# Optimization experiments

Measured on AMD Instinct MI355X. Metric: run time of the kernel, lower is better.

Reference implementation:

```python
import jax, jax.numpy as jnp
import numpy as np

SDF_W = 7000.0
EIK_W = 600.0
ORI_W = 500.0
NEAR_ORI_W = 10.0
GRADN_W = 200.0
K_NEIGHBORS = 2


def _orientation_sign(query, surface, normals, k=K_NEIGHBORS):
    # Original detaches to numpy for a scipy KDTree query -> stop_gradient here.
    q = jax.lax.stop_gradient(query)       # [Q,3]
    s = jax.lax.stop_gradient(surface)     # [S,3]
    n = jax.lax.stop_gradient(normals)     # [S,3]
    # Brute-force squared distances [Q,S] (GEMM-dominated).
    d2 = (jnp.sum(q * q, axis=-1, keepdims=True)
          - 2.0 * (q @ s.T)
          + jnp.sum(s * s, axis=-1)[None, :])
    _, idx = jax.lax.top_k(-d2, k)         # [Q,k] nearest-neighbor indices
    near_pts = s[idx]                      # [Q,k,3]
    near_nrm = n[idx]                      # [Q,k,3]
    vecs = q[:, None, :] - near_pts        # [Q,k,3]
    dots = jnp.sum(vecs * near_nrm, axis=-1)  # [Q,k]
    return jnp.sign(jnp.mean(dots, axis=1))   # [Q]


def setup_inputs() -> dict:
    key = jax.random.key(0)
    ks = jax.random.split(key, 8)
    N = 16384
    return {
        "manifold_pred": jax.random.normal(ks[0], (N, 1), jnp.float32) * 0.1,
        "manifold_grad": jax.random.normal(ks[1], (N, 3), jnp.float32),
        "nonmanifold_pred": jax.random.normal(ks[2], (N, 1), jnp.float32),
        "near_points_pred": jax.random.normal(ks[3], (N, 1), jnp.float32) * 0.1,
        "surface_points": jax.random.normal(ks[4], (N, 3), jnp.float32),
        "surface_normals": jax.random.normal(ks[5], (N, 3), jnp.float32),
        "off_surface_points": jax.random.normal(ks[6], (N, 3), jnp.float32) * 1.5,
        "near_points": jax.random.normal(ks[7], (N, 3), jnp.float32),
    }


def reference(manifold_pred, manifold_grad, nonmanifold_pred, near_points_pred,
              surface_points, surface_normals, off_surface_points, near_points):
    sdf_loss = jnp.mean(manifold_pred ** 2)
    eikonal_loss = jnp.mean((jnp.linalg.norm(manifold_grad, axis=-1) - 1.0) ** 2)

    signs_off = _orientation_sign(off_surface_points, surface_points, surface_normals)
    orientation_loss = jnp.mean(jax.nn.relu(-nonmanifold_pred * signs_off[:, None]))

    signs_near = _orientation_sign(near_points, surface_points, surface_normals)
    near_surface_orientation_loss = jnp.mean(jax.nn.relu(-near_points_pred * signs_near[:, None]))

    gradient_normal_loss = jnp.mean((manifold_grad - surface_normals) ** 2)

    total = (SDF_W * sdf_loss + EIK_W * eikonal_loss + ORI_W * orientation_loss
             + NEAR_ORI_W * near_surface_orientation_loss + GRADN_W * gradient_normal_loss)
    return (total, sdf_loss, eikonal_loss, orientation_loss,
            near_surface_orientation_loss, gradient_normal_loss)
```

## Files before the change

### kernel.cpp

```cpp
#include <hip/hip_runtime.h>
#include <math.h>

#define SDF_W      7000.0f
#define EIK_W      600.0f
#define ORI_W      500.0f
#define NEAR_ORI_W 10.0f
#define GRADN_W    200.0f

#define TILE   2048
#define NWAVE  8
#define CHK    64
#define WS_STRIDE 512
#define WS_REC 4096


__device__ __forceinline__ float neg_half_norm2(float sx, float sy, float sz) {
    return -0.5f * fmaf(sx, sx, fmaf(sy, sy, sz * sz));
}
__device__ __forceinline__ float score(float qx, float qy, float qz,
                                       float sx, float sy, float sz, float nh) {
    return fmaf(qx, sx, fmaf(qy, sy, fmaf(qz, sz, nh)));
}

__global__ __launch_bounds__(512) void nn_scan(
    const float* __restrict__ offq, const float* __restrict__ nearq,
    const float* __restrict__ surf,
    float* __restrict__ ws, int S, int Qoff, int QT)
{
    __shared__ float4 tile[TILE];
    const int t    = threadIdx.x;
    const int lane = t & 63;
    const int wv   = __builtin_amdgcn_readfirstlane(t >> 6);

    const int qgroup = blockIdx.x >> 1;
    const int shalf  = blockIdx.x & 1;

    const int halfLen = (((S + 1) / 2) + (CHK - 1)) & ~(CHK - 1);
    const int sb = shalf ? (halfLen < S ? halfLen : S) : 0;
    const int se = shalf ? S : (halfLen < S ? halfLen : S);

    const int qA = qgroup * 128 + lane;
    const int qB = qA + 64;
    float qAx = 0.f, qAy = 0.f, qAz = 0.f, qBx = 0.f, qBy = 0.f, qBz = 0.f;
    if (qA < QT) {
        const float* p = (qA < Qoff) ? (offq + 3 * qA) : (nearq + 3 * (qA - Qoff));
        qAx = p[0]; qAy = p[1]; qAz = p[2];
    }
    if (qB < QT) {
        const float* p = (qB < Qoff) ? (offq + 3 * qB) : (nearq + 3 * (qB - Qoff));
        qBx = p[0]; qBy = p[1]; qBz = p[2];
    }

    float M1a = -3.0e38f, M2a = -3.0e38f, M1b = -3.0e38f, M2b = -3.0e38f;
    float P1a = M1a, P2a = M2a, P1b = M1b, P2b = M2b;
    int c1a = 0, c2a = 0, c1b = 0, c2b = 0;

    for (int base = sb; base < se; base += TILE) {
        __syncthreads();
        {
            int p0 = base + t * 4;
            if (p0 + 4 <= se) {
                const float4* g4 = (const float4*)(surf + 3 * p0);
                float4 r0 = g4[0], r1 = g4[1], r2 = g4[2];
                tile[t*4+0] = make_float4(r0.x, r0.y, r0.z, neg_half_norm2(r0.x, r0.y, r0.z));
                tile[t*4+1] = make_float4(r0.w, r1.x, r1.y, neg_half_norm2(r0.w, r1.x, r1.y));
                tile[t*4+2] = make_float4(r1.z, r1.w, r2.x, neg_half_norm2(r1.z, r1.w, r2.x));
                tile[t*4+3] = make_float4(r2.y, r2.z, r2.w, neg_half_norm2(r2.y, r2.z, r2.w));
            } else {
                #pragma unroll
                for (int k = 0; k < 4; ++k) {
                    int p = p0 + k;
                    if (p < se) {
                        float sx = surf[3*p], sy = surf[3*p+1], sz = surf[3*p+2];
                        tile[t*4+k] = make_float4(sx, sy, sz, neg_half_norm2(sx, sy, sz));
                    } else {
                        tile[t*4+k] = make_float4(0.f, 0.f, 0.f, -3.0e38f);
                    }
                }
            }
        }
        __syncthreads();
        const int lo = wv * (TILE / NWAVE);
        const float4* tp = tile + lo;
        const int ccbase = (base + lo) >> 6;
        #pragma unroll 1
        for (int c4 = 0; c4 < (TILE / NWAVE) / CHK; ++c4) {
            const float4* cp = tp + c4 * CHK;
            #pragma unroll 8
            for (int o = 0; o < CHK; ++o) {
                float4 s4 = cp[o];
                float ga = score(qAx, qAy, qAz, s4.x, s4.y, s4.z, s4.w);
                float ta = fminf(ga, M1a);
                M2a = fmaxf(M2a, ta);
                M1a = fmaxf(M1a, ga);
                float gb = score(qBx, qBy, qBz, s4.x, s4.y, s4.z, s4.w);
                float tb = fminf(gb, M1b);
                M2b = fmaxf(M2b, tb);
                M1b = fmaxf(M1b, gb);
            }
            int cid = ccbase + c4;
            c1a = (M1a != P1a) ? cid : c1a;  P1a = M1a;
            c2a = (M2a != P2a) ? cid : c2a;  P2a = M2a;
            c1b = (M1b != P1b) ? cid : c1b;  P1b = M1b;
            c2b = (M2b != P2b) ? cid : c2b;  P2b = M2b;
        }
    }

    __syncthreads();
    float4* rec = tile;
    rec[wv * 128 + lane]      = make_float4(M1a, M2a, __int_as_float(c1a), __int_as_float(c2a));
    rec[wv * 128 + 64 + lane] = make_float4(M1b, M2b, __int_as_float(c1b), __int_as_float(c2b));
    __syncthreads();
    if (t < 128) {
        float4 r = rec[t];
        float M1 = r.x, M2 = r.y;
        int c1 = __float_as_int(r.z), c2 = __float_as_int(r.w);
        #pragma unroll
        for (int w = 1; w < NWAVE; ++w) {
            float4 a = rec[w * 128 + t];
            float a1 = a.x, a2 = a.y;
            int ac1 = __float_as_int(a.z), ac2 = __float_as_int(a.w);
            if (a1 > M1)      { M2 = M1; c2 = c1; M1 = a1; c1 = ac1; }
            else if (a1 > M2) { M2 = a1; c2 = ac1; }
            if (a2 > M2)      { M2 = a2; c2 = ac2; }
        }
        int gq = qgroup * 128 + t;
        if (gq < QT) {
            ((float4*)(ws + WS_REC))[gq * 2 + shalf] =
                make_float4(M1, M2, __int_as_float(c1), __int_as_float(c2));
        }
    }
}

__device__ __forceinline__ int find_first(const float* __restrict__ surf, int S,
                                          int c, float qx, float qy, float qz,
                                          float target, int exclude)
{
    int j0 = c * CHK;
    int j1 = j0 + CHK; if (j1 > S) j1 = S;
    if (j1 - j0 == CHK) {
        const float4* g4 = (const float4*)(surf + 3 * j0);
        int found = -1;
        #pragma unroll 1
        for (int b = 0; b < CHK / 16 && found < 0; ++b) {
            float4 raw[12];
            #pragma unroll
            for (int k = 0; k < 12; ++k) raw[k] = g4[b * 12 + k];
            const float* f = (const float*)raw;
            #pragma unroll
            for (int p = 0; p < 16; ++p) {
                float sx = f[3*p], sy = f[3*p+1], sz = f[3*p+2];
                float g = score(qx, qy, qz, sx, sy, sz, neg_half_norm2(sx, sy, sz));
                int j = j0 + b * 16 + p;
                if (found < 0 && g == target && j != exclude) found = j;
            }
        }
        return found;
    }
    for (int j = j0; j < j1; ++j) {
        float sx = surf[3*j], sy = surf[3*j+1], sz = surf[3*j+2];
        float g = score(qx, qy, qz, sx, sy, sz, neg_half_norm2(sx, sy, sz));
        if (g == target && j != exclude) return j;
    }
    return -1;
}

__global__ __launch_bounds__(128) void recover_k(
    const float* __restrict__ offq, const float* __restrict__ nearq,
    const float* __restrict__ surf, const float* __restrict__ norms,
    const float* __restrict__ nmpred, const float* __restrict__ nppred,
    const float* __restrict__ mp, const float* __restrict__ mg,
    const float* __restrict__ sn,
    float* __restrict__ ws, int S, int Qoff, int QT, int N)
{
    const int t = threadIdx.x;
    const int q = blockIdx.x * 128 + t;

    float termOri = 0.f, termNori = 0.f;
    if (q < QT) {
        const float4* recs = (const float4*)(ws + WS_REC);
        float4 r0 = recs[q * 2 + 0], r1 = recs[q * 2 + 1];
        float M1 = r0.x, M2 = r0.y;
        int c1 = __float_as_int(r0.z), c2 = __float_as_int(r0.w);
        {
            float a1 = r1.x, a2 = r1.y;
            int ac1 = __float_as_int(r1.z), ac2 = __float_as_int(r1.w);
            if (a1 > M1)      { M2 = M1; c2 = c1; M1 = a1; c1 = ac1; }
            else if (a1 > M2) { M2 = a1; c2 = ac1; }
            if (a2 > M2)      { M2 = a2; c2 = ac2; }
        }
        bool isNear = (q >= Qoff);
        const float* qp = isNear ? (nearq + 3 * (q - Qoff)) : (offq + 3 * q);
        float qx = qp[0], qy = qp[1], qz = qp[2];

        int I1 = find_first(surf, S, c1, qx, qy, qz, M1, -1);
        if (I1 < 0) I1 = 0;
        int I2 = find_first(surf, S, c2, qx, qy, qz, M2, I1);
        if (I2 < 0) I2 = (I1 == 0 && S > 1) ? 1 : 0;

        float d1 = (qx - surf[3*I1]) * norms[3*I1]
                 + (qy - surf[3*I1+1]) * norms[3*I1+1]
                 + (qz - surf[3*I1+2]) * norms[3*I1+2];
        float d2 = (qx - surf[3*I2]) * norms[3*I2]
                 + (qy - surf[3*I2+1]) * norms[3*I2+1]
                 + (qz - surf[3*I2+2]) * norms[3*I2+2];
        float ms = d1 + d2;
        float sgn = (ms > 0.f) ? 1.f : ((ms < 0.f) ? -1.f : 0.f);
        float pred = isNear ? nppred[q - Qoff] : nmpred[q];
        float term = fmaxf(0.f, -pred * sgn);
        termOri  = isNear ? 0.f : term;
        termNori = isNear ? term : 0.f;
    }

    float sdf = 0.f, eik = 0.f, gn = 0.f;
    for (int i = q; i < N; i += QT) {
        float p = mp[i];
        sdf += p * p;
        float gx = mg[3*i], gy = mg[3*i+1], gz = mg[3*i+2];
        float nrm = sqrtf(fmaf(gx, gx, fmaf(gy, gy, gz * gz)));
        float d = nrm - 1.0f;
        eik += d * d;
        float nx = sn[3*i], ny = sn[3*i+1], nz = sn[3*i+2];
        float dx = gx - nx, dy = gy - ny, dz = gz - nz;
        gn += fmaf(dx, dx, fmaf(dy, dy, dz * dz));
    }

    __shared__ float red[5][128];
    red[0][t] = termOri; red[1][t] = termNori;
    red[2][t] = sdf;     red[3][t] = eik;      red[4][t] = gn;
    __syncthreads();
    for (int off = 64; off > 0; off >>= 1) {
        if (t < off) {
            #pragma unroll
            for (int k = 0; k < 5; ++k) red[k][t] += red[k][t + off];
        }
        __syncthreads();
    }
    if (t == 0) {
        #pragma unroll
        for (int k = 0; k < 5; ++k) ws[k * WS_STRIDE + blockIdx.x] = red[k][0];
    }
}

__global__ __launch_bounds__(256) void final_k(
    const float* __restrict__ ws, float* __restrict__ out,
    int N, int RB, int Qoff, int Qnear)
{
    __shared__ float r[5][256];
    int t = threadIdx.x;
    float s[5] = {0.f, 0.f, 0.f, 0.f, 0.f};
    for (int i = t; i < RB; i += 256) {
        #pragma unroll
        for (int k = 0; k < 5; ++k) s[k] += ws[k * WS_STRIDE + i];
    }
    #pragma unroll
    for (int k = 0; k < 5; ++k) r[k][t] = s[k];
    __syncthreads();
    for (int off = 128; off > 0; off >>= 1) {
        if (t < off) {
            #pragma unroll
            for (int k = 0; k < 5; ++k) r[k][t] += r[k][t + off];
        }
        __syncthreads();
    }
    if (t == 0) {
        float orim  = r[0][0] / (float)Qoff;
        float norim = r[1][0] / (float)Qnear;
        float sdfm  = r[2][0] / (float)N;
        float eikm  = r[3][0] / (float)N;
        float gnm   = r[4][0] / (3.0f * (float)N);
        out[0] = SDF_W * sdfm + EIK_W * eikm + ORI_W * orim
               + NEAR_ORI_W * norim + GRADN_W * gnm;
        out[1] = sdfm;
        out[2] = eikm;
        out[3] = orim;
        out[4] = norim;
        out[5] = gnm;
    }
}

extern "C" void kernel_launch(void* const* d_in, const int* in_sizes, int n_in,
                              void* d_out, int out_size, void* d_ws, size_t ws_size,
                              hipStream_t stream)
{
    const float* mp    = (const float*)d_in[0];
    const float* mg    = (const float*)d_in[1];
    const float* nmp   = (const float*)d_in[2];
    const float* npp   = (const float*)d_in[3];
    const float* sp    = (const float*)d_in[4];
    const float* sn    = (const float*)d_in[5];
    const float* offp  = (const float*)d_in[6];
    const float* nearp = (const float*)d_in[7];
    float* out = (float*)d_out;

    const int N     = in_sizes[0];
    const int S     = in_sizes[4] / 3;
    const int Qoff  = in_sizes[2];
    const int Qnear = in_sizes[3];
    const int QT    = Qoff + Qnear;

    float* ws = (float*)d_ws;

    const int qgroups = (QT + 127) / 128;
    const int RB      = (QT + 127) / 128;

    nn_scan<<<qgroups * 2, 512, 0, stream>>>(offp, nearp, sp, ws, S, Qoff, QT);
    recover_k<<<RB, 128, 0, stream>>>(offp, nearp, sp, sn, nmp, npp,
                                      mp, mg, sn, ws, S, Qoff, QT, N);
    final_k<<<1, 256, 0, stream>>>(ws, out, N, RB, Qoff, Qnear);
}
```

Before: 151.1 us.

## Scan four queries per lane with fmed3 top-2 and wave-parallel index recovery

The NN scan kernel now holds four query points per lane instead of two, so each shared-memory surface load is reused across more queries. The top-2 update is compressed into a single fmed3 plus a max. Recovery now gives each query a whole wavefront, which scores the 64 chunk candidates in parallel and selects the match by ballot instead of a serial per-thread search. The block reductions use wave shuffles. The risks are higher register pressure in the scan and half as many scan blocks (256 instead of 512), which lowers occupancy and CU coverage.

```diff
diff --git a/kernel.cpp b/kernel.cpp
--- a/kernel.cpp
+++ b/kernel.cpp
@@ -10,8 +10,10 @@
 #define TILE   2048
 #define NWAVE  8
 #define CHK    64
-#define WS_STRIDE 512
-#define WS_REC 4096
+#define QPL    4
+#define QB     (QPL * 64)
+#define WS_STRIDE 8192
+#define WS_REC 65536
 
 
 __device__ __forceinline__ float neg_half_norm2(float sx, float sy, float sz) {
@@ -20,6 +22,14 @@
 __device__ __forceinline__ float score(float qx, float qy, float qz,
                                        float sx, float sy, float sz, float nh) {
     return fmaf(qx, sx, fmaf(qy, sy, fmaf(qz, sz, nh)));
+}
+
+__device__ __forceinline__ float dot_at(const float* __restrict__ surf,
+                                        const float* __restrict__ norms, int j,
+                                        float qx, float qy, float qz) {
+    float sx = surf[3*j], sy = surf[3*j+1], sz = surf[3*j+2];
+    float nx = norms[3*j], ny = norms[3*j+1], nz = norms[3*j+2];
+    return fmaf(qx - sx, nx, fmaf(qy - sy, ny, (qz - sz) * nz));
 }
 
 __global__ __launch_bounds__(512) void nn_scan(
@@ -39,21 +49,26 @@
     const int sb = shalf ? (halfLen < S ? halfLen : S) : 0;
     const int se = shalf ? S : (halfLen < S ? halfLen : S);
 
-    const int qA = qgroup * 128 + lane;
-    const int qB = qA + 64;
-    float qAx = 0.f, qAy = 0.f, qAz = 0.f, qBx = 0.f, qBy = 0.f, qBz = 0.f;
-    if (qA < QT) {
-        const float* p = (qA < Qoff) ? (offq + 3 * qA) : (nearq + 3 * (qA - Qoff));
-        qAx = p[0]; qAy = p[1]; qAz = p[2];
-    }
-    if (qB < QT) {
-        const float* p = (qB < Qoff) ? (offq + 3 * qB) : (nearq + 3 * (qB - Qoff));
-        qBx = p[0]; qBy = p[1]; qBz = p[2];
-    }
-
-    float M1a = -3.0e38f, M2a = -3.0e38f, M1b = -3.0e38f, M2b = -3.0e38f;
-    float P1a = M1a, P2a = M2a, P1b = M1b, P2b = M2b;
-    int c1a = 0, c2a = 0, c1b = 0, c2b = 0;
+    const int qbase = qgroup * QB;
+    float qx[QPL], qy[QPL], qz[QPL];
+    #pragma unroll
+    for (int j = 0; j < QPL; ++j) {
+        int q = qbase + j * 64 + lane;
+        qx[j] = 0.f; qy[j] = 0.f; qz[j] = 0.f;
+        if (q < QT) {
+            const float* p = (q < Qoff) ? (offq + 3 * q) : (nearq + 3 * (q - Qoff));
+            qx[j] = p[0]; qy[j] = p[1]; qz[j] = p[2];
+        }
+    }
+
+    float M1[QPL], M2[QPL], P1[QPL], P2[QPL];
+    int c1[QPL], c2[QPL];
+    #pragma unroll
+    for (int j = 0; j < QPL; ++j) {
+        M1[j] = -3.0e38f; M2[j] = -3.0e38f;
+        P1[j] = -3.0e38f; P2[j] = -3.0e38f;
+        c1[j] = 0; c2[j] = 0;
+    }
 
     for (int base = sb; base < se; base += TILE) {
         __syncthreads();
@@ -89,83 +104,51 @@
             #pragma unroll 8
             for (int o = 0; o < CHK; ++o) {
                 float4 s4 = cp[o];
-                float ga = score(qAx, qAy, qAz, s4.x, s4.y, s4.z, s4.w);
-                float ta = fminf(ga, M1a);
-                M2a = fmaxf(M2a, ta);
-                M1a = fmaxf(M1a, ga);
-                float gb = score(qBx, qBy, qBz, s4.x, s4.y, s4.z, s4.w);
-                float tb = fminf(gb, M1b);
-                M2b = fmaxf(M2b, tb);
-                M1b = fmaxf(M1b, gb);
+                #pragma unroll
+                for (int j = 0; j < QPL; ++j) {
+                    float g = score(qx[j], qy[j], qz[j], s4.x, s4.y, s4.z, s4.w);
+                    M2[j] = __builtin_amdgcn_fmed3f(g, M1[j], M2[j]);
+                    M1[j] = fmaxf(M1[j], g);
+                }
             }
             int cid = ccbase + c4;
-            c1a = (M1a != P1a) ? cid : c1a;  P1a = M1a;
-            c2a = (M2a != P2a) ? cid : c2a;  P2a = M2a;
-            c1b = (M1b != P1b) ? cid : c1b;  P1b = M1b;
-            c2b = (M2b != P2b) ? cid : c2b;  P2b = M2b;
+            #pragma unroll
+            for (int j = 0; j < QPL; ++j) {
+                c1[j] = (M1[j] != P1[j]) ? cid : c1[j];  P1[j] = M1[j];
+                c2[j] = (M2[j] != P2[j]) ? cid : c2[j];  P2[j] = M2[j];
+            }
         }
     }
 
     __syncthreads();
     float4* rec = tile;
-    rec[wv * 128 + lane]      = make_float4(M1a, M2a, __int_as_float(c1a), __int_as_float(c2a));
-    rec[wv * 128 + 64 + lane] = make_float4(M1b, M2b, __int_as_float(c1b), __int_as_float(c2b));
+    #pragma unroll
+    for (int j = 0; j < QPL; ++j)
+        rec[wv * QB + j * 64 + lane] =
+            make_float4(M1[j], M2[j], __int_as_float(c1[j]), __int_as_float(c2[j]));
     __syncthreads();
-    if (t < 128) {
+    if (t < QB) {
         float4 r = rec[t];
-        float M1 = r.x, M2 = r.y;
-        int c1 = __float_as_int(r.z), c2 = __float_as_int(r.w);
+        float m1 = r.x, m2 = r.y;
+        int k1 = __float_as_int(r.z), k2 = __float_as_int(r.w);
         #pragma unroll
         for (int w = 1; w < NWAVE; ++w) {
-            float4 a = rec[w * 128 + t];
+            float4 a = rec[w * QB + t];
             float a1 = a.x, a2 = a.y;
             int ac1 = __float_as_int(a.z), ac2 = __float_as_int(a.w);
-            if (a1 > M1)      { M2 = M1; c2 = c1; M1 = a1; c1 = ac1; }
-            else if (a1 > M2) { M2 = a1; c2 = ac1; }
-            if (a2 > M2)      { M2 = a2; c2 = ac2; }
-        }
-        int gq = qgroup * 128 + t;
+            if (a1 > m1)      { m2 = m1; k2 = k1; m1 = a1; k1 = ac1; }
+            else if (a1 > m2) { m2 = a1; k2 = ac1; }
+            if (a2 > m2)      { m2 = a2; k2 = ac2; }
+        }
+        int gq = qbase + t;
         if (gq < QT) {
             ((float4*)(ws + WS_REC))[gq * 2 + shalf] =
-                make_float4(M1, M2, __int_as_float(c1), __int_as_float(c2));
-        }
-    }
-}
-
-__device__ __forceinline__ int find_first(const float* __restrict__ surf, int S,
-                                          int c, float qx, float qy, float qz,
-                                          float target, int exclude)
-{
-    int j0 = c * CHK;
-    int j1 = j0 + CHK; if (j1 > S) j1 = S;
-    if (j1 - j0 == CHK) {
-        const float4* g4 = (const float4*)(surf + 3 * j0);
-        int found = -1;
-        #pragma unroll 1
-        for (int b = 0; b < CHK / 16 && found < 0; ++b) {
-            float4 raw[12];
-            #pragma unroll
-            for (int k = 0; k < 12; ++k) raw[k] = g4[b * 12 + k];
-            const float* f = (const float*)raw;
-            #pragma unroll
-            for (int p = 0; p < 16; ++p) {
-                float sx = f[3*p], sy = f[3*p+1], sz = f[3*p+2];
-                float g = score(qx, qy, qz, sx, sy, sz, neg_half_norm2(sx, sy, sz));
-                int j = j0 + b * 16 + p;
-                if (found < 0 && g == target && j != exclude) found = j;
-            }
-        }
-        return found;
-    }
-    for (int j = j0; j < j1; ++j) {
-        float sx = surf[3*j], sy = surf[3*j+1], sz = surf[3*j+2];
-        float g = score(qx, qy, qz, sx, sy, sz, neg_half_norm2(sx, sy, sz));
-        if (g == target && j != exclude) return j;
-    }
-    return -1;
-}
-
-__global__ __launch_bounds__(128) void recover_k(
+                make_float4(m1, m2, __int_as_float(k1), __int_as_float(k2));
+        }
+    }
+}
+
+__global__ __launch_bounds__(512) void recover_k(
     const float* __restrict__ offq, const float* __restrict__ nearq,
     const float* __restrict__ surf, const float* __restrict__ norms,
     const float* __restrict__ nmpred, const float* __restrict__ nppred,
@@ -173,8 +156,10 @@
     const float* __restrict__ sn,
     float* __restrict__ ws, int S, int Qoff, int QT, int N)
 {
-    const int t = threadIdx.x;
-    const int q = blockIdx.x * 128 + t;
+    const int t    = threadIdx.x;
+    const int lane = t & 63;
+    const int wv   = t >> 6;
+    const int q    = blockIdx.x * 8 + wv;
 
     float termOri = 0.f, termNori = 0.f;
     if (q < QT) {
@@ -193,27 +178,58 @@
         const float* qp = isNear ? (nearq + 3 * (q - Qoff)) : (offq + 3 * q);
         float qx = qp[0], qy = qp[1], qz = qp[2];
 
-        int I1 = find_first(surf, S, c1, qx, qy, qz, M1, -1);
-        if (I1 < 0) I1 = 0;
-        int I2 = find_first(surf, S, c2, qx, qy, qz, M2, I1);
-        if (I2 < 0) I2 = (I1 == 0 && S > 1) ? 1 : 0;
-
-        float d1 = (qx - surf[3*I1]) * norms[3*I1]
-                 + (qy - surf[3*I1+1]) * norms[3*I1+1]
-                 + (qz - surf[3*I1+2]) * norms[3*I1+2];
-        float d2 = (qx - surf[3*I2]) * norms[3*I2]
-                 + (qy - surf[3*I2+1]) * norms[3*I2+1]
-                 + (qz - surf[3*I2+2]) * norms[3*I2+2];
+        int j1 = c1 * CHK + lane;
+        float g1 = -3.0e38f, dot1 = 0.f;
+        if (j1 < S) {
+            float sx = surf[3*j1], sy = surf[3*j1+1], sz = surf[3*j1+2];
+            g1 = score(qx, qy, qz, sx, sy, sz, neg_half_norm2(sx, sy, sz));
+            float nx = norms[3*j1], ny = norms[3*j1+1], nz = norms[3*j1+2];
+            dot1 = fmaf(qx - sx, nx, fmaf(qy - sy, ny, (qz - sz) * nz));
+        }
+        unsigned long long m1mask = __ballot(g1 == M1);
+        int I1; float d1;
+        if (m1mask) {
+            int l1 = __ffsll(m1mask) - 1;
+            I1 = c1 * CHK + l1;
+            d1 = __shfl(dot1, l1);
+        } else {
+            I1 = 0;
+            d1 = dot_at(surf, norms, 0, qx, qy, qz);
+        }
+
+        int j2 = c2 * CHK + lane;
+        float g2 = -3.0e38f, dot2 = 0.f;
+        if (j2 < S) {
+            float sx = surf[3*j2], sy = surf[3*j2+1], sz = surf[3*j2+2];
+            g2 = score(qx, qy, qz, sx, sy, sz, neg_half_norm2(sx, sy, sz));
+            float nx = norms[3*j2], ny = norms[3*j2+1], nz = norms[3*j2+2];
+            dot2 = fmaf(qx - sx, nx, fmaf(qy - sy, ny, (qz - sz) * nz));
+        }
+        unsigned long long m2mask = __ballot(g2 == M2);
+        int rel = I1 - c2 * CHK;
+        if (rel >= 0 && rel < 64) m2mask &= ~(1ull << rel);
+        int I2; float d2;
+        if (m2mask) {
+            int l2 = __ffsll(m2mask) - 1;
+            I2 = c2 * CHK + l2;
+            d2 = __shfl(dot2, l2);
+        } else {
+            I2 = (I1 == 0 && S > 1) ? 1 : 0;
+            d2 = dot_at(surf, norms, I2, qx, qy, qz);
+        }
+
         float ms = d1 + d2;
         float sgn = (ms > 0.f) ? 1.f : ((ms < 0.f) ? -1.f : 0.f);
         float pred = isNear ? nppred[q - Qoff] : nmpred[q];
         float term = fmaxf(0.f, -pred * sgn);
-        termOri  = isNear ? 0.f : term;
-        termNori = isNear ? term : 0.f;
+        if (lane == 0) {
+            termOri  = isNear ? 0.f : term;
+            termNori = isNear ? term : 0.f;
+        }
     }
 
     float sdf = 0.f, eik = 0.f, gn = 0.f;
-    for (int i = q; i < N; i += QT) {
+    for (int i = blockIdx.x * 512 + t; i < N; i += gridDim.x * 512) {
         float p = mp[i];
         sdf += p * p;
         float gx = mg[3*i], gy = mg[3*i+1], gz = mg[3*i+2];
@@ -225,20 +241,29 @@
         gn += fmaf(dx, dx, fmaf(dy, dy, dz * dz));
     }
 
-    __shared__ float red[5][128];
-    red[0][t] = termOri; red[1][t] = termNori;
-    red[2][t] = sdf;     red[3][t] = eik;      red[4][t] = gn;
+    float v0 = termOri, v1 = termNori, v2 = sdf, v3 = eik, v4 = gn;
+    #pragma unroll
+    for (int off = 32; off > 0; off >>= 1) {
+        v0 += __shfl_down(v0, off);
+        v1 += __shfl_down(v1, off);
+        v2 += __shfl_down(v2, off);
+        v3 += __shfl_down(v3, off);
+        v4 += __shfl_down(v4, off);
+    }
+    __shared__ float red[5][NWAVE];
+    if (lane == 0) {
+        red[0][wv] = v0; red[1][wv] = v1; red[2][wv] = v2;
+        red[3][wv] = v3; red[4][wv] = v4;
+    }
     __syncthreads();
-    for (int off = 64; off > 0; off >>= 1) {
-        if (t < off) {
-            #pragma unroll
-            for (int k = 0; k < 5; ++k) red[k][t] += red[k][t + off];
-        }
-        __syncthreads();
-    }
     if (t == 0) {
         #pragma unroll
-        for (int k = 0; k < 5; ++k) ws[k * WS_STRIDE + blockIdx.x] = red[k][0];
+        for (int k = 0; k < 5; ++k) {
+            float s = 0.f;
+            #pragma unroll
+            for (int w = 0; w < NWAVE; ++w) s += red[k][w];
+            ws[k * WS_STRIDE + blockIdx.x] = s;
+        }
     }
 }
 
@@ -301,11 +326,11 @@
 
     float* ws = (float*)d_ws;
 
-    const int qgroups = (QT + 127) / 128;
-    const int RB      = (QT + 127) / 128;
+    const int qgroups = (QT + QB - 1) / QB;
+    const int RB      = (QT + 7) / 8;
 
     nn_scan<<<qgroups * 2, 512, 0, stream>>>(offp, nearp, sp, ws, S, Qoff, QT);
-    recover_k<<<RB, 128, 0, stream>>>(offp, nearp, sp, sn, nmp, npp,
+    recover_k<<<RB, 512, 0, stream>>>(offp, nearp, sp, sn, nmp, npp,
                                       mp, mg, sn, ws, S, Qoff, QT, N);
     final_k<<<1, 256, 0, stream>>>(ws, out, N, RB, Qoff, Qnear);
 }
```

After: 170.0 us. +12.6%, slower.
